# Kernel optimization log

Hardware: AMD Instinct MI355X
Metric: run time of the kernel (lower is better)

## Reference

```python
import jax, jax.numpy as jnp
import numpy as np

NUM_HEADS = 16
HEAD_DIM = 64  # hidden 1024 / 16 heads


def setup_inputs() -> dict:
    key = jax.random.key(0)
    ks = jax.random.split(key, 4)
    B, S, D = 2, 2048, 1024
    scale = 1.0 / np.sqrt(D)
    return {
        "hidden_states": jax.random.normal(ks[0], (B, S, D), jnp.float32),
        "Wq": jax.random.normal(ks[1], (D, D), jnp.float32) * scale,
        "bq": jnp.zeros((D,), jnp.float32),
        "Wk": jax.random.normal(ks[2], (D, D), jnp.float32) * scale,
        "bk": jnp.zeros((D,), jnp.float32),
        "Wv": jax.random.normal(ks[3], (D, D), jnp.float32) * scale,
        "bv": jnp.zeros((D,), jnp.float32),
    }


def _split_heads(x):
    B, S, D = x.shape
    return x.reshape(B, S, NUM_HEADS, HEAD_DIM).transpose(0, 2, 1, 3)  # [B,H,S,dh]


def reference(hidden_states, Wq, bq, Wk, bk, Wv, bv):
    q = _split_heads(hidden_states @ Wq + bq)
    k = _split_heads(hidden_states @ Wk + bk)
    v = _split_heads(hidden_states @ Wv + bv)
    scores = jnp.einsum("bhqd,bhkd->bhqk", q, k) / jnp.sqrt(
        jnp.asarray(HEAD_DIM, hidden_states.dtype))
    probs = jax.nn.softmax(scores, axis=-1)  # dropout is identity in eval mode
    ctx = jnp.einsum("bhqk,bhkd->bhqd", probs, v)
    B, H, S, dh = ctx.shape
    return ctx.transpose(0, 2, 1, 3).reshape(B, S, H * dh)
```

## Files before the change

### kernel.cpp

```cpp
#include <hip/hip_runtime.h>
#include <hip/hip_bf16.h>


typedef __attribute__((ext_vector_type(8))) short bf16x8;
typedef __attribute__((ext_vector_type(4))) float f32x4;
typedef __attribute__((ext_vector_type(4))) int int4v;

#define MFMA16(A, B, C) __builtin_amdgcn_mfma_f32_16x16x32_bf16((A), (B), (C), 0, 0, 0)

#if __has_builtin(__builtin_amdgcn_exp2f)
#define EXP2(x) __builtin_amdgcn_exp2f(x)
#else
#define EXP2(x) exp2f(x)
#endif

static __device__ __forceinline__ unsigned short f2bf(float f) {
    union { float f; unsigned int u; } v;
    v.f = f;
    unsigned int u = v.u;
    u += ((u >> 16) & 1u) + 0x7FFFu;
    return (unsigned short)(u >> 16);
}

static __device__ __forceinline__ unsigned short f2bf_hw(float f) {
    __hip_bfloat16 h = __float2bfloat16(f);
    return *reinterpret_cast<unsigned short*>(&h);
}

static __device__ __forceinline__ void gload_lds16(const void* g, void* l) {
    __builtin_amdgcn_global_load_lds(
        (const __attribute__((address_space(1))) void*)g,
        (__attribute__((address_space(3))) void*)l, 16, 0, 0);
}

__global__ __launch_bounds__(256) void cast_hs(const float* __restrict__ in,
                                               unsigned short* __restrict__ out) {
    const size_t i = ((size_t)blockIdx.x * 256 + threadIdx.x) * 8;
    float4 a0 = *reinterpret_cast<const float4*>(in + i);
    float4 a1 = *reinterpret_cast<const float4*>(in + i + 4);
    unsigned short t[8];
    t[0] = f2bf(a0.x); t[1] = f2bf(a0.y); t[2] = f2bf(a0.z); t[3] = f2bf(a0.w);
    t[4] = f2bf(a1.x); t[5] = f2bf(a1.y); t[6] = f2bf(a1.z); t[7] = f2bf(a1.w);
    *reinterpret_cast<int4v*>(out + i) = *reinterpret_cast<int4v*>(t);
}

__global__ __launch_bounds__(256) void transpose_cast_w(
    const float* __restrict__ W0, const float* __restrict__ W1,
    const float* __restrict__ W2, unsigned short* __restrict__ Wt) {
    __shared__ float Ts[64][65];
    const float* W = (blockIdx.z == 0) ? W0 : (blockIdx.z == 1) ? W1 : W2;
    unsigned short* O = Wt + (size_t)blockIdx.z * 1048576;

    const int t  = threadIdx.x;
    const int k0 = blockIdx.y * 64;
    const int n0 = blockIdx.x * 64;

    {
        const int kr = t >> 2, nc = (t & 3) * 16;
        const float* p = W + (size_t)(k0 + kr) * 1024 + n0 + nc;
        float4 r0 = *reinterpret_cast<const float4*>(p);
        float4 r1 = *reinterpret_cast<const float4*>(p + 4);
        float4 r2 = *reinterpret_cast<const float4*>(p + 8);
        float4 r3 = *reinterpret_cast<const float4*>(p + 12);
        float* d = &Ts[kr][nc];
        d[0]=r0.x; d[1]=r0.y; d[2]=r0.z; d[3]=r0.w;
        d[4]=r1.x; d[5]=r1.y; d[6]=r1.z; d[7]=r1.w;
        d[8]=r2.x; d[9]=r2.y; d[10]=r2.z; d[11]=r2.w;
        d[12]=r3.x; d[13]=r3.y; d[14]=r3.z; d[15]=r3.w;
    }
    __syncthreads();
    {
        const int nr = t >> 2, kc = (t & 3) * 16;
        unsigned short tmp[16];
#pragma unroll
        for (int i = 0; i < 16; i++) tmp[i] = f2bf(Ts[kc + i][nr]);
        unsigned short* d = O + (size_t)(n0 + nr) * 1024 + k0 + kc;
        *reinterpret_cast<int4v*>(d)     = *reinterpret_cast<int4v*>(&tmp[0]);
        *reinterpret_cast<int4v*>(d + 8) = *reinterpret_cast<int4v*>(&tmp[8]);
    }
}

__global__ __launch_bounds__(256) void qkv_gemm_dma(
    const unsigned short* __restrict__ hsb,
    const unsigned short* __restrict__ Wt,
    const float* __restrict__ b0, const float* __restrict__ b1,
    const float* __restrict__ b2,
    unsigned short* __restrict__ Qo,
    unsigned short* __restrict__ Ko,
    unsigned short* __restrict__ Vto)
{
    __shared__ unsigned short As[128][32];
    __shared__ unsigned short Bs[128][32];

    const int z = blockIdx.z;
    const unsigned short* W = Wt + (size_t)z * 1048576;
    const float* bias = (z == 0) ? b0 : (z == 1) ? b1 : b2;

    const int tid  = threadIdx.x;
    const int lane = tid & 63;
    const int w    = tid >> 6;
    const int l15  = lane & 15;
    const int quad = lane >> 4;
    const int m0   = blockIdx.y * 128;
    const int n0   = blockIdx.x * 128;
    const int wm   = (w >> 1) * 64;
    const int wn   = (w & 1) * 64;

    const int drow = lane >> 2;
    const int dcol = (lane & 3) * 8;

    f32x4 acc[4][4];
#pragma unroll
    for (int i = 0; i < 4; i++)
#pragma unroll
        for (int j = 0; j < 4; j++)
            acc[i][j] = (f32x4){0.f, 0.f, 0.f, 0.f};

    for (int k0 = 0; k0 < 1024; k0 += 32) {
        __syncthreads();
#pragma unroll
        for (int p = 0; p < 2; p++) {
            const int s = w * 2 + p;
            gload_lds16(hsb + (size_t)(m0 + s * 16 + drow) * 1024 + k0 + dcol,
                        &As[s * 16][0]);
            gload_lds16(W   + (size_t)(n0 + s * 16 + drow) * 1024 + k0 + dcol,
                        &Bs[s * 16][0]);
        }
        __syncthreads();

        bf16x8 af[4], bfr[4];
#pragma unroll
        for (int i = 0; i < 4; i++)
            af[i] = *reinterpret_cast<const bf16x8*>(&As[wm + i * 16 + l15][quad * 8]);
#pragma unroll
        for (int j = 0; j < 4; j++)
            bfr[j] = *reinterpret_cast<const bf16x8*>(&Bs[wn + j * 16 + l15][quad * 8]);
#pragma unroll
        for (int i = 0; i < 4; i++)
#pragma unroll
            for (int j = 0; j < 4; j++)
                acc[i][j] = MFMA16(af[i], bfr[j], acc[i][j]);
    }

    if (z == 0) {
        const float qs = 0.18033688f;
#pragma unroll
        for (int i = 0; i < 4; i++) {
            const int mbase = m0 + wm + i * 16 + quad * 4;
#pragma unroll
            for (int j = 0; j < 4; j++) {
                const int n = n0 + wn + j * 16 + l15;
                const int h = n >> 6, d = n & 63;
                const float bn = bias[n];
#pragma unroll
                for (int r = 0; r < 4; r++) {
                    const int mm = mbase + r;
                    const int b = mm >> 11, s = mm & 2047;
                    Qo[(((size_t)(b * 16 + h) * 2048 + s) * 64) + d] =
                        f2bf((acc[i][j][r] + bn) * qs);
                }
            }
        }
    } else if (z == 1) {
#pragma unroll
        for (int i = 0; i < 4; i++) {
            const int mbase = m0 + wm + i * 16 + quad * 4;
#pragma unroll
            for (int j = 0; j < 4; j++) {
                const int n = n0 + wn + j * 16 + l15;
                const int h = n >> 6, d = n & 63;
                const float bn = bias[n];
#pragma unroll
                for (int r = 0; r < 4; r++) {
                    const int mm = mbase + r;
                    const int b = mm >> 11, s = mm & 2047;
                    const int dsw = ((((d >> 3) ^ (s & 7)) & 7) << 3) | (d & 7);
                    Ko[(((size_t)(b * 16 + h) * 2048 + s) * 64) + dsw] =
                        f2bf(acc[i][j][r] + bn);
                }
            }
        }
    } else {
#pragma unroll
        for (int i = 0; i < 4; i++) {
            const int mbase = m0 + wm + i * 16 + quad * 4;
            const int b = mbase >> 11, s0 = mbase & 2047;
#pragma unroll
            for (int j = 0; j < 4; j++) {
                const int n = n0 + wn + j * 16 + l15;
                const int h = n >> 6, d = n & 63;
                const float bn = bias[n];
                ushort4 v4;
                v4.x = f2bf(acc[i][j][0] + bn);
                v4.y = f2bf(acc[i][j][1] + bn);
                v4.z = f2bf(acc[i][j][2] + bn);
                v4.w = f2bf(acc[i][j][3] + bn);
                const int cs  = (s0 & 63) >> 3;
                const int ssw = (s0 & ~63) | (((cs ^ (d & 7)) & 7) << 3) | (s0 & 7);
                *reinterpret_cast<ushort4*>(
                    Vto + ((size_t)(b * 16 + h) * 64 + d) * 2048 + ssw) = v4;
            }
        }
    }
}

__global__ __launch_bounds__(512) void attn3(
    const unsigned short* __restrict__ Qg,
    const unsigned short* __restrict__ Kg,
    const unsigned short* __restrict__ Vtg,
    float* __restrict__ out)
{
    __shared__ unsigned short Ks[2][64][64];
    __shared__ unsigned short Vs[2][64][64];
    __shared__ unsigned short Ps[8][16][68];

    const int tid  = threadIdx.x;
    const int lane = tid & 63;
    const int w    = tid >> 6;
    const int l15  = lane & 15;
    const int quad = lane >> 4;

    const int lin = blockIdx.x;
    const int qb  = (lin >> 3) & 15;
    const int bh  = (lin & 7) | ((lin >> 7) << 3);
    const int q0  = qb * 128;
    const size_t base = (size_t)bh * 2048 * 64;
    const unsigned short* Qh  = Qg  + base;
    const unsigned short* Kh  = Kg  + base;
    const unsigned short* Vth = Vtg + base;
    const int b = bh >> 4;
    const int h = bh & 15;

    const int drow = lane >> 3;
    const int dcol = (lane & 7) * 8;

    bf16x8 qf[2];
#pragma unroll
    for (int ks = 0; ks < 2; ks++)
        qf[ks] = *reinterpret_cast<const bf16x8*>(
            Qh + (size_t)(q0 + w * 16 + l15) * 64 + ks * 32 + quad * 8);

    f32x4 o[4];
#pragma unroll
    for (int t = 0; t < 4; t++) o[t] = (f32x4){0.f, 0.f, 0.f, 0.f};
    float rsum[4] = {0.f, 0.f, 0.f, 0.f};

    const int c0 = (((quad + 0) ^ (l15 & 7)) & 7) * 8;
    const int c1 = (((quad + 4) ^ (l15 & 7)) & 7) * 8;

    gload_lds16(Kh  + (size_t)(w * 8 + drow) * 64 + dcol,   &Ks[0][w * 8][0]);
    gload_lds16(Vth + (size_t)(w * 8 + drow) * 2048 + dcol, &Vs[0][w * 8][0]);
    __syncthreads();

    int cur = 0;
    for (int kt = 0; kt < 32; kt++) {
        if (kt < 31) {
            const int kn = kt + 1;
            gload_lds16(Kh  + (size_t)kn * 4096 + (size_t)(w * 8 + drow) * 64 + dcol,
                        &Ks[cur ^ 1][w * 8][0]);
            gload_lds16(Vth + (size_t)(w * 8 + drow) * 2048 + kn * 64 + dcol,
                        &Vs[cur ^ 1][w * 8][0]);
        }

        const unsigned short (*Kc)[64] = Ks[cur];
        const unsigned short (*Vc)[64] = Vs[cur];

#pragma unroll
        for (int t = 0; t < 4; t++) {
            f32x4 sc = (f32x4){0.f, 0.f, 0.f, 0.f};
            bf16x8 kf0 = *reinterpret_cast<const bf16x8*>(&Kc[t * 16 + l15][c0]);
            bf16x8 kf1 = *reinterpret_cast<const bf16x8*>(&Kc[t * 16 + l15][c1]);
            __builtin_amdgcn_s_setprio(1);
            sc = MFMA16(qf[0], kf0, sc);
            sc = MFMA16(qf[1], kf1, sc);
            __builtin_amdgcn_s_setprio(0);
#pragma unroll
            for (int r = 0; r < 4; r++) {
                const float p = EXP2(sc[r]);
                rsum[r] += p;
                Ps[w][quad * 4 + r][t * 16 + l15] = f2bf_hw(p);
            }
        }

        asm volatile("s_waitcnt lgkmcnt(0)" ::: "memory");
        __builtin_amdgcn_sched_barrier(0);

        bf16x8 pf[2];
#pragma unroll
        for (int ks = 0; ks < 2; ks++)
            pf[ks] = *reinterpret_cast<const bf16x8*>(&Ps[w][l15][ks * 32 + quad * 8]);

#pragma unroll
        for (int t = 0; t < 4; t++) {
            bf16x8 vf0 = *reinterpret_cast<const bf16x8*>(&Vc[t * 16 + l15][c0]);
            bf16x8 vf1 = *reinterpret_cast<const bf16x8*>(&Vc[t * 16 + l15][c1]);
            __builtin_amdgcn_s_setprio(1);
            o[t] = MFMA16(pf[0], vf0, o[t]);
            o[t] = MFMA16(pf[1], vf1, o[t]);
            __builtin_amdgcn_s_setprio(0);
        }

        __syncthreads();
        cur ^= 1;
    }

#pragma unroll
    for (int off = 1; off < 16; off <<= 1)
#pragma unroll
        for (int r = 0; r < 4; r++)
            rsum[r] += __shfl_xor(rsum[r], off, 64);

#pragma unroll
    for (int t = 0; t < 4; t++) {
#pragma unroll
        for (int r = 0; r < 4; r++) {
            const int q = q0 + w * 16 + quad * 4 + r;
            const size_t oidx = (((size_t)b * 2048 + q) * 16 + h) * 64 + t * 16 + l15;
            out[oidx] = o[t][r] / rsum[r];
        }
    }
}

__global__ void fill_sentinel(float* out, int n, float pat) {
    int i = blockIdx.x * blockDim.x + threadIdx.x;
    if (i < n) out[i] = pat;
}

extern "C" void kernel_launch(void* const* d_in, const int* in_sizes, int n_in,
                              void* d_out, int out_size, void* d_ws, size_t ws_size,
                              hipStream_t stream) {
    const size_t n_hs  = (size_t)4096 * 1024;
    const size_t n_w   = (size_t)1024 * 1024;
    const size_t n_qkv = n_hs;
    const size_t need = (n_hs + 3 * n_w + 3 * n_qkv) * sizeof(unsigned short);

    bool order_ok = (n_in == 7) &&
        in_sizes[0] == 4194304 &&
        in_sizes[1] == 1048576 && in_sizes[2] == 1024 &&
        in_sizes[3] == 1048576 && in_sizes[4] == 1024 &&
        in_sizes[5] == 1048576 && in_sizes[6] == 1024;
    if (!order_ok || out_size != 4194304) {
        fill_sentinel<<<(out_size + 255) / 256, 256, 0, stream>>>(
            (float*)d_out, out_size, 4.0f);
        return;
    }
    if (ws_size < need) {
        fill_sentinel<<<(out_size + 255) / 256, 256, 0, stream>>>(
            (float*)d_out, out_size, 2.0f);
        return;
    }

    const float* hs = (const float*)d_in[0];
    const float* Wq = (const float*)d_in[1];
    const float* bq = (const float*)d_in[2];
    const float* Wk = (const float*)d_in[3];
    const float* bk = (const float*)d_in[4];
    const float* Wv = (const float*)d_in[5];
    const float* bv = (const float*)d_in[6];

    unsigned short* hsb = (unsigned short*)d_ws;
    unsigned short* Wt  = hsb + n_hs;
    unsigned short* Q   = Wt + 3 * n_w;
    unsigned short* K   = Q + n_qkv;
    unsigned short* Vt  = K + n_qkv;

    cast_hs<<<2048, 256, 0, stream>>>(hs, hsb);
    transpose_cast_w<<<dim3(16, 16, 3), 256, 0, stream>>>(Wq, Wk, Wv, Wt);

    dim3 g1(8, 32, 3);
    qkv_gemm_dma<<<g1, dim3(256), 0, stream>>>(hsb, Wt, bq, bk, bv, Q, K, Vt);

    attn3<<<dim3(512), dim3(512), 0, stream>>>(Q, K, Vt, (float*)d_out);
}
```

Baseline: 188.2 us.

## Process two 16-row query groups per wave to reuse K/V fragments

Each wave now handles 32 query rows (two groups of 16) instead of 16, so each block covers 256 queries and the grid halves to 256 blocks. K and V fragments are loaded from LDS once per tile and reused across both query groups, which halves LDS reads and global K/V traffic per query. In exchange, register pressure rises and there are only 256 blocks for the CUs, which can leave some CUs idle and reduce latency hiding.

```diff
diff --git a/kernel.cpp b/kernel.cpp
--- a/kernel.cpp
+++ b/kernel.cpp
@@ -221,9 +221,9 @@
     const int quad = lane >> 4;
 
     const int lin = blockIdx.x;
-    const int qb  = (lin >> 3) & 15;
-    const int bh  = (lin & 7) | ((lin >> 7) << 3);
-    const int q0  = qb * 128;
+    const int qb  = (lin >> 3) & 7;
+    const int bh  = (lin & 7) | ((lin >> 6) << 3);
+    const int q0  = qb * 256;
     const size_t base = (size_t)bh * 2048 * 64;
     const unsigned short* Qh  = Qg  + base;
     const unsigned short* Kh  = Kg  + base;
@@ -234,16 +234,20 @@
     const int drow = lane >> 3;
     const int dcol = (lane & 7) * 8;
 
-    bf16x8 qf[2];
-#pragma unroll
-    for (int ks = 0; ks < 2; ks++)
-        qf[ks] = *reinterpret_cast<const bf16x8*>(
-            Qh + (size_t)(q0 + w * 16 + l15) * 64 + ks * 32 + quad * 8);
-
-    f32x4 o[4];
-#pragma unroll
-    for (int t = 0; t < 4; t++) o[t] = (f32x4){0.f, 0.f, 0.f, 0.f};
-    float rsum[4] = {0.f, 0.f, 0.f, 0.f};
+    bf16x8 qf[2][2];
+#pragma unroll
+    for (int g = 0; g < 2; g++)
+#pragma unroll
+        for (int ks = 0; ks < 2; ks++)
+            qf[g][ks] = *reinterpret_cast<const bf16x8*>(
+                Qh + (size_t)(q0 + w * 32 + g * 16 + l15) * 64 + ks * 32 + quad * 8);
+
+    f32x4 o[2][4];
+#pragma unroll
+    for (int g = 0; g < 2; g++)
+#pragma unroll
+        for (int t = 0; t < 4; t++) o[g][t] = (f32x4){0.f, 0.f, 0.f, 0.f};
+    float rsum[2][4] = {{0.f, 0.f, 0.f, 0.f}, {0.f, 0.f, 0.f, 0.f}};
 
     const int c0 = (((quad + 0) ^ (l15 & 7)) & 7) * 8;
     const int c1 = (((quad + 4) ^ (l15 & 7)) & 7) * 8;
@@ -265,39 +269,48 @@
         const unsigned short (*Kc)[64] = Ks[cur];
         const unsigned short (*Vc)[64] = Vs[cur];
 
+        bf16x8 kf[4][2], vf[4][2];
 #pragma unroll
         for (int t = 0; t < 4; t++) {
-            f32x4 sc = (f32x4){0.f, 0.f, 0.f, 0.f};
-            bf16x8 kf0 = *reinterpret_cast<const bf16x8*>(&Kc[t * 16 + l15][c0]);
-            bf16x8 kf1 = *reinterpret_cast<const bf16x8*>(&Kc[t * 16 + l15][c1]);
-            __builtin_amdgcn_s_setprio(1);
-            sc = MFMA16(qf[0], kf0, sc);
-            sc = MFMA16(qf[1], kf1, sc);
-            __builtin_amdgcn_s_setprio(0);
-#pragma unroll
-            for (int r = 0; r < 4; r++) {
-                const float p = EXP2(sc[r]);
-                rsum[r] += p;
-                Ps[w][quad * 4 + r][t * 16 + l15] = f2bf_hw(p);
-            }
-        }
-
-        asm volatile("s_waitcnt lgkmcnt(0)" ::: "memory");
-        __builtin_amdgcn_sched_barrier(0);
-
-        bf16x8 pf[2];
-#pragma unroll
-        for (int ks = 0; ks < 2; ks++)
-            pf[ks] = *reinterpret_cast<const bf16x8*>(&Ps[w][l15][ks * 32 + quad * 8]);
-
-#pragma unroll
-        for (int t = 0; t < 4; t++) {
-            bf16x8 vf0 = *reinterpret_cast<const bf16x8*>(&Vc[t * 16 + l15][c0]);
-            bf16x8 vf1 = *reinterpret_cast<const bf16x8*>(&Vc[t * 16 + l15][c1]);
-            __builtin_amdgcn_s_setprio(1);
-            o[t] = MFMA16(pf[0], vf0, o[t]);
-            o[t] = MFMA16(pf[1], vf1, o[t]);
-            __builtin_amdgcn_s_setprio(0);
+            kf[t][0] = *reinterpret_cast<const bf16x8*>(&Kc[t * 16 + l15][c0]);
+            kf[t][1] = *reinterpret_cast<const bf16x8*>(&Kc[t * 16 + l15][c1]);
+            vf[t][0] = *reinterpret_cast<const bf16x8*>(&Vc[t * 16 + l15][c0]);
+            vf[t][1] = *reinterpret_cast<const bf16x8*>(&Vc[t * 16 + l15][c1]);
+        }
+
+#pragma unroll
+        for (int g = 0; g < 2; g++) {
+#pragma unroll
+            for (int t = 0; t < 4; t++) {
+                f32x4 sc = (f32x4){0.f, 0.f, 0.f, 0.f};
+                __builtin_amdgcn_s_setprio(1);
+                sc = MFMA16(qf[g][0], kf[t][0], sc);
+                sc = MFMA16(qf[g][1], kf[t][1], sc);
+                __builtin_amdgcn_s_setprio(0);
+#pragma unroll
+                for (int r = 0; r < 4; r++) {
+                    const float p = EXP2(sc[r]);
+                    rsum[g][r] += p;
+                    Ps[w][quad * 4 + r][t * 16 + l15] = f2bf_hw(p);
+                }
+            }
+
+            asm volatile("s_waitcnt lgkmcnt(0)" ::: "memory");
+            __builtin_amdgcn_sched_barrier(0);
+
+            bf16x8 pf[2];
+#pragma unroll
+            for (int ks = 0; ks < 2; ks++)
+                pf[ks] = *reinterpret_cast<const bf16x8*>(
+                    &Ps[w][l15][ks * 32 + quad * 8]);
+
+#pragma unroll
+            for (int t = 0; t < 4; t++) {
+                __builtin_amdgcn_s_setprio(1);
+                o[g][t] = MFMA16(pf[0], vf[t][0], o[g][t]);
+                o[g][t] = MFMA16(pf[1], vf[t][1], o[g][t]);
+                __builtin_amdgcn_s_setprio(0);
+            }
         }
 
         __syncthreads();
@@ -307,18 +320,22 @@
 #pragma unroll
     for (int off = 1; off < 16; off <<= 1)
 #pragma unroll
-        for (int r = 0; r < 4; r++)
-            rsum[r] += __shfl_xor(rsum[r], off, 64);
-
-#pragma unroll
-    for (int t = 0; t < 4; t++) {
-#pragma unroll
-        for (int r = 0; r < 4; r++) {
-            const int q = q0 + w * 16 + quad * 4 + r;
-            const size_t oidx = (((size_t)b * 2048 + q) * 16 + h) * 64 + t * 16 + l15;
-            out[oidx] = o[t][r] / rsum[r];
-        }
-    }
+        for (int g = 0; g < 2; g++)
+#pragma unroll
+            for (int r = 0; r < 4; r++)
+                rsum[g][r] += __shfl_xor(rsum[g][r], off, 64);
+
+#pragma unroll
+    for (int g = 0; g < 2; g++)
+#pragma unroll
+        for (int t = 0; t < 4; t++)
+#pragma unroll
+            for (int r = 0; r < 4; r++) {
+                const int q = q0 + w * 32 + g * 16 + quad * 4 + r;
+                const size_t oidx =
+                    (((size_t)b * 2048 + q) * 16 + h) * 64 + t * 16 + l15;
+                out[oidx] = o[g][t][r] / rsum[g][r];
+            }
 }
 
 __global__ void fill_sentinel(float* out, int n, float pat) {
@@ -370,5 +387,5 @@
     dim3 g1(8, 32, 3);
     qkv_gemm_dma<<<g1, dim3(256), 0, stream>>>(hsb, Wt, bq, bk, bv, Q, K, Vt);
 
-    attn3<<<dim3(512), dim3(512), 0, stream>>>(Q, K, Vt, (float*)d_out);
-}
+    attn3<<<dim3(256), dim3(512), 0, stream>>>(Q, K, Vt, (float*)d_out);
+}
```

Result: slower. 192.2 us (+2.1%).

## Keep softmax probabilities in registers via transposed QK^T and permlane swaps

Applied to the files above, without the earlier changes.

Computes the score tile transposed (K as the A operand) so each lane holds four consecutive key columns for one query row. The probabilities are packed to bf16 pairs and rearranged into the P·V operand layout with v_permlane32/16 swaps, so the per-wave LDS P buffer and its lgkmcnt wait are no longer needed. Row sums now accumulate per lane and are reduced across lane groups at the end, then redistributed with shuffles. It relies on gfx950 permlane swap instructions and on the lane mapping being exactly right.

```diff
diff --git a/kernel.cpp b/kernel.cpp
--- a/kernel.cpp
+++ b/kernel.cpp
@@ -25,6 +25,10 @@
 static __device__ __forceinline__ unsigned short f2bf_hw(float f) {
     __hip_bfloat16 h = __float2bfloat16(f);
     return *reinterpret_cast<unsigned short*>(&h);
+}
+
+static __device__ __forceinline__ unsigned int pack2(float lo, float hi) {
+    return ((unsigned int)f2bf_hw(hi) << 16) | (unsigned int)f2bf_hw(lo);
 }
 
 static __device__ __forceinline__ void gload_lds16(const void* g, void* l) {
@@ -212,7 +216,6 @@
 {
     __shared__ unsigned short Ks[2][64][64];
     __shared__ unsigned short Vs[2][64][64];
-    __shared__ unsigned short Ps[8][16][68];
 
     const int tid  = threadIdx.x;
     const int lane = tid & 63;
@@ -243,7 +246,7 @@
     f32x4 o[4];
 #pragma unroll
     for (int t = 0; t < 4; t++) o[t] = (f32x4){0.f, 0.f, 0.f, 0.f};
-    float rsum[4] = {0.f, 0.f, 0.f, 0.f};
+    float rsum = 0.f;
 
     const int c0 = (((quad + 0) ^ (l15 & 7)) & 7) * 8;
     const int c1 = (((quad + 4) ^ (l15 & 7)) & 7) * 8;
@@ -265,30 +268,38 @@
         const unsigned short (*Kc)[64] = Ks[cur];
         const unsigned short (*Vc)[64] = Vs[cur];
 
+        unsigned int D[4][2];
 #pragma unroll
         for (int t = 0; t < 4; t++) {
             f32x4 sc = (f32x4){0.f, 0.f, 0.f, 0.f};
             bf16x8 kf0 = *reinterpret_cast<const bf16x8*>(&Kc[t * 16 + l15][c0]);
             bf16x8 kf1 = *reinterpret_cast<const bf16x8*>(&Kc[t * 16 + l15][c1]);
             __builtin_amdgcn_s_setprio(1);
-            sc = MFMA16(qf[0], kf0, sc);
-            sc = MFMA16(qf[1], kf1, sc);
+            sc = MFMA16(kf0, qf[0], sc);
+            sc = MFMA16(kf1, qf[1], sc);
             __builtin_amdgcn_s_setprio(0);
-#pragma unroll
-            for (int r = 0; r < 4; r++) {
-                const float p = EXP2(sc[r]);
-                rsum[r] += p;
-                Ps[w][quad * 4 + r][t * 16 + l15] = f2bf_hw(p);
-            }
-        }
-
-        asm volatile("s_waitcnt lgkmcnt(0)" ::: "memory");
-        __builtin_amdgcn_sched_barrier(0);
+            const float p0 = EXP2(sc[0]);
+            const float p1 = EXP2(sc[1]);
+            const float p2 = EXP2(sc[2]);
+            const float p3 = EXP2(sc[3]);
+            rsum += (p0 + p1) + (p2 + p3);
+            D[t][0] = pack2(p0, p1);
+            D[t][1] = pack2(p2, p3);
+        }
 
         bf16x8 pf[2];
 #pragma unroll
-        for (int ks = 0; ks < 2; ks++)
-            pf[ks] = *reinterpret_cast<const bf16x8*>(&Ps[w][l15][ks * 32 + quad * 8]);
+        for (int ks = 0; ks < 2; ks++) {
+            unsigned int x0 = D[2 * ks][0], y0 = D[2 * ks + 1][0];
+            unsigned int x1 = D[2 * ks][1], y1 = D[2 * ks + 1][1];
+            asm("v_permlane32_swap_b32 %0, %1" : "+v"(x0), "+v"(y0));
+            asm("v_permlane16_swap_b32 %0, %1" : "+v"(x0), "+v"(y0));
+            asm("v_permlane32_swap_b32 %0, %1" : "+v"(x1), "+v"(y1));
+            asm("v_permlane16_swap_b32 %0, %1" : "+v"(x1), "+v"(y1));
+            int4v pv_;
+            pv_.x = (int)x0; pv_.y = (int)x1; pv_.z = (int)y0; pv_.w = (int)y1;
+            pf[ks] = *reinterpret_cast<bf16x8*>(&pv_);
+        }
 
 #pragma unroll
         for (int t = 0; t < 4; t++) {
@@ -304,11 +315,12 @@
         cur ^= 1;
     }
 
-#pragma unroll
-    for (int off = 1; off < 16; off <<= 1)
-#pragma unroll
-        for (int r = 0; r < 4; r++)
-            rsum[r] += __shfl_xor(rsum[r], off, 64);
+    rsum += __shfl_xor(rsum, 16, 64);
+    rsum += __shfl_xor(rsum, 32, 64);
+    float rq[4];
+#pragma unroll
+    for (int r = 0; r < 4; r++)
+        rq[r] = __shfl(rsum, quad * 4 + r, 64);
 
 #pragma unroll
     for (int t = 0; t < 4; t++) {
@@ -316,7 +328,7 @@
         for (int r = 0; r < 4; r++) {
             const int q = q0 + w * 16 + quad * 4 + r;
             const size_t oidx = (((size_t)b * 2048 + q) * 16 + h) * 64 + t * 16 + l15;
-            out[oidx] = o[t][r] / rsum[r];
+            out[oidx] = o[t][r] / rq[r];
         }
     }
 }
```

New measurement: 182.2 us. 3.2% less time.
